# Performance work log

Measured on AMD Instinct MI355X. Metric: run time of the kernel, lower is better.

## Reference

```python
import jax, jax.numpy as jnp
import numpy as np

B, L, D_MODEL = 2, 2048, 1024
EXPAND, D_STATE, D_CONV = 2, 16, 4
D_INNER = EXPAND * D_MODEL
DT_RANK = D_MODEL // 16  # mamba default: ceil(d_model/16)


def setup_inputs() -> dict:
    key = jax.random.key(0)
    ks = jax.random.split(key, 8)
    s = 0.02
    return {
        "x": jax.random.normal(ks[0], (B, L, D_MODEL), jnp.float32),
        "in_proj_w": jax.random.normal(ks[1], (2 * D_INNER, D_MODEL), jnp.float32) * s,
        "conv_w": jax.random.normal(ks[2], (D_INNER, D_CONV), jnp.float32) * s,
        "conv_b": jnp.zeros((D_INNER,), jnp.float32),
        "x_proj_w": jax.random.normal(ks[3], (DT_RANK + 2 * D_STATE, D_INNER), jnp.float32) * s,
        "dt_proj_w": jax.random.normal(ks[4], (D_INNER, DT_RANK), jnp.float32) * s,
        "dt_proj_b": jnp.full((D_INNER,), -4.6, jnp.float32),  # softplus(-4.6) ~ 0.01 dt init
        "A_log": jnp.log(jnp.broadcast_to(jnp.arange(1, D_STATE + 1, dtype=jnp.float32), (D_INNER, D_STATE))),
        "D": jnp.ones((D_INNER,), jnp.float32),
        "ssm_out_w": jax.random.normal(ks[5], (D_MODEL, D_INNER), jnp.float32) * s,
        "final_w": jax.random.normal(ks[6], (D_MODEL, D_MODEL), jnp.float32) * s,
        "final_b": jnp.zeros((D_MODEL,), jnp.float32),
    }


def _forward(x, in_proj_w, conv_w, conv_b, x_proj_w, dt_proj_w, dt_proj_b,
             A_log, D, ssm_out_w, final_w, final_b):
    d_inner, d_state = A_log.shape
    dt_rank = dt_proj_w.shape[1]
    d_conv = conv_w.shape[1]

    # in_proj -> split into x-branch and gate z  (B, L, 2*d_inner)
    xz = jnp.einsum('bld,ed->ble', x, in_proj_w)
    xin, z = jnp.split(xz, 2, axis=-1)

    # causal depthwise conv1d over time, then SiLU
    xc = jax.lax.conv_general_dilated(
        xin.swapaxes(1, 2),               # (B, d_inner, L)
        conv_w[:, None, :],               # (O=d_inner, I/g=1, W=d_conv)
        window_strides=(1,),
        padding=[(d_conv - 1, 0)],
        dimension_numbers=('NCH', 'OIH', 'NCH'),
        feature_group_count=d_inner,
    )
    xc = jax.nn.silu(xc + conv_b[None, :, None]).swapaxes(1, 2)  # (B, L, d_inner)

    # input-dependent SSM parameters
    x_dbl = jnp.einsum('bld,ed->ble', xc, x_proj_w)              # (B, L, dt_rank+2*d_state)
    dt, Bm, Cm = jnp.split(x_dbl, [dt_rank, dt_rank + d_state], axis=-1)
    delta = jax.nn.softplus(jnp.einsum('blr,dr->bld', dt, dt_proj_w) + dt_proj_b)  # (B,L,d_inner)
    A = -jnp.exp(A_log)                                          # (d_inner, d_state)

    # selective scan: h_t = exp(dt*A) h_{t-1} + dt*B_t*u_t ; y_t = <h_t, C_t>
    def step(h, t):
        delta_t, B_t, C_t, u_t = t                               # (B,Di), (B,N), (B,N), (B,Di)
        h = jnp.exp(delta_t[..., None] * A) * h + (delta_t * u_t)[..., None] * B_t[:, None, :]
        return h, jnp.einsum('bdn,bn->bd', h, C_t)

    h0 = jnp.zeros((x.shape[0], d_inner, d_state), x.dtype)
    xs = (delta.swapaxes(0, 1), Bm.swapaxes(0, 1), Cm.swapaxes(0, 1), xc.swapaxes(0, 1))
    _, ys = jax.lax.scan(step, h0, xs)                           # (L, B, d_inner)

    y = ys.swapaxes(0, 1) + xc * D                               # skip term D*u
    y = y * jax.nn.silu(z)                                       # gating
    out = jnp.einsum('bld,md->blm', y, ssm_out_w)                # Mamba out_proj -> d_model
    # wrapper: Linear(d_model, d_model) then SiLU
    return jax.nn.silu(jnp.einsum('blm,nm->bln', out, final_w) + final_b)


def reference(x, in_proj_w, conv_w, conv_b, x_proj_w, dt_proj_w, dt_proj_b,
              A_log, D, ssm_out_w, final_w, final_b):
    return _forward(x, in_proj_w, conv_w, conv_b, x_proj_w, dt_proj_w, dt_proj_b,
                    A_log, D, ssm_out_w, final_w, final_b)
```

## Files before the change

kernel.cpp:

```cpp
#include <hip/hip_runtime.h>
#include <hip/hip_bf16.h>
#include <math.h>

#define BB 2
#define LL 2048
#define DMODEL 1024
#define DINNER 2048
#define DSTATE 16
#define DCONV 4
#define DTRANK 64
#define MROWS (BB * LL)
#define XPROJ_N (DTRANK + 2 * DSTATE)

#define SEG 64
#define LS (LL / SEG)
#define DPB 64

#define XKSPLIT 8
#define XKC (DINNER / XKSPLIT)

typedef unsigned short ushort_t;
typedef short s8v __attribute__((ext_vector_type(8)));
typedef float f4v __attribute__((ext_vector_type(4)));

__device__ __forceinline__ float siluf(float x) {
    return x / (1.f + expf(-x));
}
__device__ __forceinline__ float softplusf(float x) {
    return fmaxf(x, 0.f) + log1pf(expf(-fabsf(x)));
}
__device__ __forceinline__ ushort_t f32_to_bf16(float f) {
    unsigned u = __builtin_bit_cast(unsigned, f);
    unsigned r = (u + 0x7FFFu + ((u >> 16) & 1u)) >> 16;
    return (ushort_t)r;
}
__device__ __forceinline__ float bf16_to_f32(ushort_t u) {
    return __builtin_bit_cast(float, ((unsigned)u) << 16);
}

__global__ __launch_bounds__(256) void prep_kernel(
    const float* __restrict__ x, const float* __restrict__ ipw,
    const float* __restrict__ sow, const float* __restrict__ fw,
    const float* __restrict__ xpw, const float* __restrict__ dtw,
    ushort_t* __restrict__ x_bf, ushort_t* __restrict__ ipw_bf,
    ushort_t* __restrict__ sow_bf, ushort_t* __restrict__ fw_bf,
    ushort_t* __restrict__ xpw_bf, ushort_t* __restrict__ dtw_bf,
    float4* __restrict__ xdbl_zero)
{
    const long i = ((long)blockIdx.x * 256 + threadIdx.x) * 4;
    const float* src; ushort_t* dst; long off;
    if      (i < 4194304L)  { src = x;   dst = x_bf;   off = i; }
    else if (i < 8388608L)  { src = ipw; dst = ipw_bf; off = i - 4194304L; }
    else if (i < 10485760L) { src = sow; dst = sow_bf; off = i - 8388608L; }
    else if (i < 11534336L) { src = fw;  dst = fw_bf;  off = i - 10485760L; }
    else if (i < 11730944L) { src = xpw; dst = xpw_bf; off = i - 11534336L; }
    else if (i < 11862016L) { src = dtw; dst = dtw_bf; off = i - 11730944L; }
    else { xdbl_zero[(i - 11862016L) >> 2] = make_float4(0.f, 0.f, 0.f, 0.f); return; }
    const float4 v = *reinterpret_cast<const float4*>(src + off);
    ushort_t o[4] = {f32_to_bf16(v.x), f32_to_bf16(v.y),
                     f32_to_bf16(v.z), f32_to_bf16(v.w)};
    *reinterpret_cast<uint2*>(dst + off) = *reinterpret_cast<uint2*>(o);
}

__global__ __launch_bounds__(256) void cast_dt_kernel(
    const float* __restrict__ xdbl, ushort_t* __restrict__ dtbf)
{
    const int i4 = (blockIdx.x * 256 + threadIdx.x) * 4;
    const int row = i4 >> 6;
    const int col = i4 & 63;
    const float4 v = *reinterpret_cast<const float4*>(&xdbl[(size_t)row * XPROJ_N + col]);
    ushort_t o[4] = {f32_to_bf16(v.x), f32_to_bf16(v.y),
                     f32_to_bf16(v.z), f32_to_bf16(v.w)};
    *reinterpret_cast<uint2*>(dtbf + i4) = *reinterpret_cast<uint2*>(o);
}

#define TM 128
#define TN 128
#define TBK 32

__global__ __launch_bounds__(512) void gemm_bf16_mfma(
    const ushort_t* __restrict__ A, int lda,
    const ushort_t* __restrict__ B, int ldb,
    int K,
    void* __restrict__ C0v, void* __restrict__ C1v, int splitN, int ldc,
    const float* __restrict__ bias, int act, int store_bf16)
{
    __shared__ __align__(16) ushort_t As[TM * TBK];
    __shared__ __align__(16) ushort_t Bs[TN * TBK];

    const int tid  = threadIdx.x;
    const int lane = tid & 63;
    const int w    = tid >> 6;
    const int wm   = w & 1;
    const int wn   = w >> 1;
    const int m0   = blockIdx.y * TM;
    const int n0   = blockIdx.x * TN;

    const int srow = lane >> 2;
    const int scol = (lane & 3) * 8;

    f4v acc[4][2] = {};

    for (int k0 = 0; k0 < K; k0 += TBK) {
        {
            const ushort_t* ga = A + (size_t)(m0 + w * 16 + srow) * lda + k0 + scol;
            __builtin_amdgcn_global_load_lds(
                (const __attribute__((address_space(1))) unsigned int*)ga,
                (__attribute__((address_space(3))) unsigned int*)(As + w * 512),
                16, 0, 0);
        }
        {
            const ushort_t* gb = B + (size_t)(n0 + w * 16 + srow) * ldb + k0 + scol;
            __builtin_amdgcn_global_load_lds(
                (const __attribute__((address_space(1))) unsigned int*)gb,
                (__attribute__((address_space(3))) unsigned int*)(Bs + w * 512),
                16, 0, 0);
        }
        __syncthreads();

        const int fr = lane & 15;
        const int kg = lane >> 4;
        s8v a[4], b[2];
        #pragma unroll
        for (int t = 0; t < 4; ++t)
            a[t] = *reinterpret_cast<const s8v*>(As + (wm * 64 + t * 16 + fr) * TBK + kg * 8);
        #pragma unroll
        for (int t = 0; t < 2; ++t)
            b[t] = *reinterpret_cast<const s8v*>(Bs + (wn * 32 + t * 16 + fr) * TBK + kg * 8);
        #pragma unroll
        for (int i = 0; i < 4; ++i)
            #pragma unroll
            for (int j = 0; j < 2; ++j)
                acc[i][j] = __builtin_amdgcn_mfma_f32_16x16x32_bf16(
                    a[i], b[j], acc[i][j], 0, 0, 0);
        __syncthreads();
    }

    const int rbase = (lane >> 4) * 4;
    const int cbase = lane & 15;
    #pragma unroll
    for (int i = 0; i < 4; ++i) {
        #pragma unroll
        for (int j = 0; j < 2; ++j) {
            const int row = m0 + wm * 64 + i * 16 + rbase;
            const int col = n0 + wn * 32 + j * 16 + cbase;
            void* Cp = C0v;
            int c2 = col;
            if (C1v && col >= splitN) { Cp = C1v; c2 = col - splitN; }
            const float bv = bias ? bias[col] : 0.f;
            #pragma unroll
            for (int r = 0; r < 4; ++r) {
                float v = acc[i][j][r] + bv;
                if (act == 1) v = siluf(v);
                else if (act == 2) v = softplusf(v);
                if (store_bf16)
                    ((ushort_t*)Cp)[(size_t)(row + r) * ldc + c2] = f32_to_bf16(v);
                else
                    ((float*)Cp)[(size_t)(row + r) * ldc + c2] = v;
            }
        }
    }
}

#define UM 64
#define UN 128

__global__ __launch_bounds__(512) void gemm64_bf16_mfma(
    const ushort_t* __restrict__ A, int lda,
    const ushort_t* __restrict__ B, int ldb,
    int K,
    void* __restrict__ C0v, int ldc,
    const float* __restrict__ bias, int act, int store_bf16)
{
    __shared__ __align__(16) ushort_t As[UM * TBK];
    __shared__ __align__(16) ushort_t Bs[UN * TBK];

    const int tid  = threadIdx.x;
    const int lane = tid & 63;
    const int w    = tid >> 6;
    const int wm   = w & 1;
    const int wn   = w >> 1;
    const int m0   = blockIdx.y * UM;
    const int n0   = blockIdx.x * UN;

    const int srow = lane >> 2;
    const int scol = (lane & 3) * 8;

    f4v acc[2][2] = {};

    for (int k0 = 0; k0 < K; k0 += TBK) {
        if (w < 4) {
            const ushort_t* ga = A + (size_t)(m0 + w * 16 + srow) * lda + k0 + scol;
            __builtin_amdgcn_global_load_lds(
                (const __attribute__((address_space(1))) unsigned int*)ga,
                (__attribute__((address_space(3))) unsigned int*)(As + w * 512),
                16, 0, 0);
        }
        {
            const ushort_t* gb = B + (size_t)(n0 + w * 16 + srow) * ldb + k0 + scol;
            __builtin_amdgcn_global_load_lds(
                (const __attribute__((address_space(1))) unsigned int*)gb,
                (__attribute__((address_space(3))) unsigned int*)(Bs + w * 512),
                16, 0, 0);
        }
        __syncthreads();

        const int fr = lane & 15;
        const int kg = lane >> 4;
        s8v a[2], b[2];
        #pragma unroll
        for (int t = 0; t < 2; ++t)
            a[t] = *reinterpret_cast<const s8v*>(As + (wm * 32 + t * 16 + fr) * TBK + kg * 8);
        #pragma unroll
        for (int t = 0; t < 2; ++t)
            b[t] = *reinterpret_cast<const s8v*>(Bs + (wn * 32 + t * 16 + fr) * TBK + kg * 8);
        #pragma unroll
        for (int i = 0; i < 2; ++i)
            #pragma unroll
            for (int j = 0; j < 2; ++j)
                acc[i][j] = __builtin_amdgcn_mfma_f32_16x16x32_bf16(
                    a[i], b[j], acc[i][j], 0, 0, 0);
        __syncthreads();
    }

    const int rbase = (lane >> 4) * 4;
    const int cbase = lane & 15;
    #pragma unroll
    for (int i = 0; i < 2; ++i) {
        #pragma unroll
        for (int j = 0; j < 2; ++j) {
            const int row = m0 + wm * 32 + i * 16 + rbase;
            const int col = n0 + wn * 32 + j * 16 + cbase;
            const float bv = bias ? bias[col] : 0.f;
            #pragma unroll
            for (int r = 0; r < 4; ++r) {
                float v = acc[i][j][r] + bv;
                if (act == 1) v = siluf(v);
                else if (act == 2) v = softplusf(v);
                if (store_bf16)
                    ((ushort_t*)C0v)[(size_t)(row + r) * ldc + col] = f32_to_bf16(v);
                else
                    ((float*)C0v)[(size_t)(row + r) * ldc + col] = v;
            }
        }
    }
}

__global__ __launch_bounds__(256) void xproj_mfma(
    const ushort_t* __restrict__ A, const ushort_t* __restrict__ Bw,
    float* __restrict__ Cout)
{
    __shared__ __align__(16) ushort_t As[64 * 32];
    __shared__ __align__(16) ushort_t Bs[96 * 32];

    const int tid = threadIdx.x;
    const int lane = tid & 63;
    const int w = tid >> 6;
    const int kbase = blockIdx.x * XKC;
    const int m0 = blockIdx.y * 64;

    const int srow = lane >> 2;
    const int scol = (lane & 3) * 8;

    f4v acc[6] = {};

    for (int k0 = kbase; k0 < kbase + XKC; k0 += 32) {
        {
            const ushort_t* ga = A + (size_t)(m0 + w * 16 + srow) * DINNER + k0 + scol;
            __builtin_amdgcn_global_load_lds(
                (const __attribute__((address_space(1))) unsigned int*)ga,
                (__attribute__((address_space(3))) unsigned int*)(As + (w * 16) * 32),
                16, 0, 0);
        }
        {
            const ushort_t* gb = Bw + (size_t)(w * 16 + srow) * DINNER + k0 + scol;
            __builtin_amdgcn_global_load_lds(
                (const __attribute__((address_space(1))) unsigned int*)gb,
                (__attribute__((address_space(3))) unsigned int*)(Bs + (w * 16) * 32),
                16, 0, 0);
        }
        if (w < 2) {
            const ushort_t* gb = Bw + (size_t)((4 + w) * 16 + srow) * DINNER + k0 + scol;
            __builtin_amdgcn_global_load_lds(
                (const __attribute__((address_space(1))) unsigned int*)gb,
                (__attribute__((address_space(3))) unsigned int*)(Bs + ((4 + w) * 16) * 32),
                16, 0, 0);
        }
        __syncthreads();

        const int fr = lane & 15;
        const int kg = lane >> 4;
        const s8v a = *reinterpret_cast<const s8v*>(As + (w * 16 + fr) * 32 + kg * 8);
        #pragma unroll
        for (int j = 0; j < 6; ++j) {
            const s8v b = *reinterpret_cast<const s8v*>(Bs + (j * 16 + fr) * 32 + kg * 8);
            acc[j] = __builtin_amdgcn_mfma_f32_16x16x32_bf16(a, b, acc[j], 0, 0, 0);
        }
        __syncthreads();
    }

    const int rbase = (lane >> 4) * 4;
    const int cb = lane & 15;
    #pragma unroll
    for (int j = 0; j < 6; ++j)
        #pragma unroll
        for (int r = 0; r < 4; ++r)
            atomicAdd(&Cout[(size_t)(m0 + w * 16 + rbase + r) * XPROJ_N + j * 16 + cb],
                      acc[j][r]);
}

__global__ __launch_bounds__(256) void conv_silu_kernel(
    const ushort_t* __restrict__ xin, const float* __restrict__ w,
    const float* __restrict__ b, ushort_t* __restrict__ xcbf)
{
    const int idx = blockIdx.x * blockDim.x + threadIdx.x;
    const int c = idx % DINNER;
    const int bl = idx / DINNER;
    const int l = bl % LL;
    const int bb = bl / LL;
    if (bb >= BB) return;

    const ushort_t* xp = xin + (size_t)bb * LL * DINNER + c;
    float acc = b[c];
    #pragma unroll
    for (int k = 0; k < DCONV; ++k) {
        const int ll = l - (DCONV - 1) + k;
        if (ll >= 0)
            acc = fmaf(bf16_to_f32(xp[(size_t)ll * DINNER]), w[c * DCONV + k], acc);
    }
    xcbf[idx] = f32_to_bf16(siluf(acc));
}

__global__ __launch_bounds__(256) void scan_part1(
    const ushort_t* __restrict__ delta, const float* __restrict__ xdbl,
    const ushort_t* __restrict__ xc, const float* __restrict__ A_log,
    float* __restrict__ hloc, float* __restrict__ decay)
{
    const int tid = threadIdx.x;
    const int nsub = tid & 3;
    const int d = blockIdx.x * DPB + (tid >> 2);
    const int seg = blockIdx.y;
    const int b = blockIdx.z;
    const int t0 = seg * LS;

    float Ad[4];
    #pragma unroll
    for (int i = 0; i < 4; ++i)
        Ad[i] = -expf(A_log[d * DSTATE + nsub * 4 + i]);

    float h[4] = {};

    const ushort_t* dp = delta + ((size_t)b * LL) * DINNER + d;
    const ushort_t* up = xc    + ((size_t)b * LL) * DINNER + d;
    const float*    xb = xdbl  + ((size_t)b * LL) * XPROJ_N;

    float sum_dl = 0.f;
    for (int t = t0; t < t0 + LS; ++t) {
        const float dl = bf16_to_f32(dp[(size_t)t * DINNER]);
        const float u  = bf16_to_f32(up[(size_t)t * DINNER]);
        const float4 Bv = *reinterpret_cast<const float4*>(
            &xb[t * XPROJ_N + DTRANK + nsub * 4]);
        const float bv[4] = {Bv.x, Bv.y, Bv.z, Bv.w};
        const float dlu = dl * u;
        sum_dl += dl;
        #pragma unroll
        for (int i = 0; i < 4; ++i)
            h[i] = __expf(dl * Ad[i]) * h[i] + dlu * bv[i];
    }

    const size_t base = (((size_t)b * SEG + seg) * DSTATE + nsub * 4) * DINNER + d;
    #pragma unroll
    for (int i = 0; i < 4; ++i) {
        hloc[base + (size_t)i * DINNER]  = h[i];
        decay[base + (size_t)i * DINNER] = __expf(Ad[i] * sum_dl);
    }
}

__global__ __launch_bounds__(256) void scan_combine(
    float* __restrict__ hloc, const float* __restrict__ decay)
{
    const int idx = blockIdx.x * 256 + threadIdx.x;
    const int d = idx % DINNER;
    const int n = (idx / DINNER) % DSTATE;
    const int b = idx / (DINNER * DSTATE);
    if (b >= BB) return;

    float carry = 0.f;
    for (int s = 0; s < SEG; ++s) {
        const size_t off = (((size_t)b * SEG + s) * DSTATE + n) * DINNER + d;
        const float hl = hloc[off];
        hloc[off] = carry;
        carry = decay[off] * carry + hl;
    }
}

__global__ __launch_bounds__(256) void scan_part2(
    const ushort_t* __restrict__ delta, const float* __restrict__ xdbl,
    const ushort_t* __restrict__ xc, const ushort_t* __restrict__ z,
    const float* __restrict__ A_log, const float* __restrict__ Dvec,
    const float* __restrict__ hstart, ushort_t* __restrict__ ybf)
{
    const int tid = threadIdx.x;
    const int nsub = tid & 3;
    const int d = blockIdx.x * DPB + (tid >> 2);
    const int seg = blockIdx.y;
    const int b = blockIdx.z;
    const int t0 = seg * LS;

    float Ad[4];
    #pragma unroll
    for (int i = 0; i < 4; ++i)
        Ad[i] = -expf(A_log[d * DSTATE + nsub * 4 + i]);

    float h[4];
    const size_t hbase = (((size_t)b * SEG + seg) * DSTATE + nsub * 4) * DINNER + d;
    #pragma unroll
    for (int i = 0; i < 4; ++i)
        h[i] = hstart[hbase + (size_t)i * DINNER];

    const float Dd = Dvec[d];
    const ushort_t* dp = delta + ((size_t)b * LL) * DINNER + d;
    const ushort_t* up = xc    + ((size_t)b * LL) * DINNER + d;
    const float*    xb = xdbl  + ((size_t)b * LL) * XPROJ_N;
    const ushort_t* zp = z     + ((size_t)b * LL) * DINNER + d;
    ushort_t*       yp = ybf   + ((size_t)b * LL) * DINNER + d;

    for (int t = t0; t < t0 + LS; ++t) {
        const float dl = bf16_to_f32(dp[(size_t)t * DINNER]);
        const float u  = bf16_to_f32(up[(size_t)t * DINNER]);
        const float zv = bf16_to_f32(zp[(size_t)t * DINNER]);
        const float4 Bv = *reinterpret_cast<const float4*>(
            &xb[t * XPROJ_N + DTRANK + nsub * 4]);
        const float4 Cv = *reinterpret_cast<const float4*>(
            &xb[t * XPROJ_N + DTRANK + DSTATE + nsub * 4]);
        const float bv[4] = {Bv.x, Bv.y, Bv.z, Bv.w};
        const float cv[4] = {Cv.x, Cv.y, Cv.z, Cv.w};
        const float dlu = dl * u;
        float y = 0.f;
        #pragma unroll
        for (int i = 0; i < 4; ++i) {
            h[i] = __expf(dl * Ad[i]) * h[i] + dlu * bv[i];
            y = fmaf(h[i], cv[i], y);
        }
        y += __shfl_xor(y, 1);
        y += __shfl_xor(y, 2);
        if (nsub == 0)
            yp[(size_t)t * DINNER] = f32_to_bf16((y + u * Dd) * siluf(zv));
    }
}

extern "C" void kernel_launch(void* const* d_in, const int* in_sizes, int n_in,
                              void* d_out, int out_size, void* d_ws, size_t ws_size,
                              hipStream_t stream) {
    const float* x         = (const float*)d_in[0];
    const float* in_proj_w = (const float*)d_in[1];
    const float* conv_w    = (const float*)d_in[2];
    const float* conv_b    = (const float*)d_in[3];
    const float* x_proj_w  = (const float*)d_in[4];
    const float* dt_proj_w = (const float*)d_in[5];
    const float* dt_proj_b = (const float*)d_in[6];
    const float* A_log     = (const float*)d_in[7];
    const float* Dvec      = (const float*)d_in[8];
    const float* ssm_out_w = (const float*)d_in[9];
    const float* final_w   = (const float*)d_in[10];
    const float* final_b   = (const float*)d_in[11];
    float* out = (float*)d_out;

    const size_t MB = 1024 * 1024;
    char* base = (char*)d_ws;
    ushort_t* xin_bf   = (ushort_t*)(base);
    ushort_t* z_bf     = (ushort_t*)(base + 16 * MB);
    ushort_t* xc_bf    = (ushort_t*)(base + 32 * MB);
    ushort_t* delta_bf = (ushort_t*)(base + 48 * MB);
    float*    xdbl     = (float*)(base + 64 * MB);
    ushort_t* x_bf     = (ushort_t*)(base + 78 * MB);
    ushort_t* ipw_bf   = (ushort_t*)(base + 86 * MB);
    ushort_t* sow_bf   = (ushort_t*)(base + 94 * MB);
    ushort_t* fw_bf    = (ushort_t*)(base + 98 * MB);
    ushort_t* xpw_bf   = (ushort_t*)(base + 100 * MB);
    ushort_t* dtw_bf   = (ushort_t*)(base + 100 * MB + 512 * 1024);
    ushort_t* dt_bf    = (ushort_t*)(base + 101 * MB);
    ushort_t* y_bf     = (ushort_t*)(base + 102 * MB);
    ushort_t* outb_bf  = (ushort_t*)(base + 118 * MB);
    float* hloc  = (float*)(base);
    float* decay = (float*)(base + 78 * MB);

    prep_kernel<<<11968, 256, 0, stream>>>(
        x, in_proj_w, ssm_out_w, final_w, x_proj_w, dt_proj_w,
        x_bf, ipw_bf, sow_bf, fw_bf, xpw_bf, dtw_bf, (float4*)xdbl);

    gemm_bf16_mfma<<<dim3(2 * DINNER / TN, MROWS / TM), 512, 0, stream>>>(
        x_bf, DMODEL, ipw_bf, DMODEL, DMODEL,
        xin_bf, z_bf, DINNER, DINNER, nullptr, 0, 1);

    conv_silu_kernel<<<(MROWS * DINNER) / 256, 256, 0, stream>>>(
        xin_bf, conv_w, conv_b, xc_bf);

    xproj_mfma<<<dim3(XKSPLIT, MROWS / 64), 256, 0, stream>>>(xc_bf, xpw_bf, xdbl);

    cast_dt_kernel<<<(MROWS * DTRANK / 4) / 256, 256, 0, stream>>>(xdbl, dt_bf);
    gemm64_bf16_mfma<<<dim3(DINNER / UN, MROWS / UM), 512, 0, stream>>>(
        dt_bf, DTRANK, dtw_bf, DTRANK, DTRANK,
        delta_bf, DINNER, dt_proj_b, 2, 1);

    scan_part1<<<dim3(DINNER / DPB, SEG, BB), 256, 0, stream>>>(
        delta_bf, xdbl, xc_bf, A_log, hloc, decay);
    scan_combine<<<(BB * DSTATE * DINNER) / 256, 256, 0, stream>>>(hloc, decay);
    scan_part2<<<dim3(DINNER / DPB, SEG, BB), 256, 0, stream>>>(
        delta_bf, xdbl, xc_bf, z_bf, A_log, Dvec, hloc, y_bf);

    gemm64_bf16_mfma<<<dim3(DMODEL / UN, MROWS / UM), 512, 0, stream>>>(
        y_bf, DINNER, sow_bf, DINNER, DINNER,
        outb_bf, DMODEL, nullptr, 0, 1);

    gemm64_bf16_mfma<<<dim3(DMODEL / UN, MROWS / UM), 512, 0, stream>>>(
        outb_bf, DMODEL, fw_bf, DMODEL, DMODEL,
        out, DMODEL, final_b, 1, 0);
}
```

Before: 417.7 us.

## Assign one thread per channel holding all 16 SSM states in registers

The chunked scan kernels change from four threads per inner channel (each owning 4 states, combined with cross-lane shuffles) to one thread per channel owning all 16 states. This removes the shuffle reduction and the redundant delta/u/z loads across the four sub-lanes, and each thread's memory accesses are coalesced per channel. In exchange the grid shrinks fourfold (8x64x2 blocks of 256 threads) and register pressure per thread rises, which lowers parallelism and occupancy.

```diff
diff --git a/kernel.cpp b/kernel.cpp
--- a/kernel.cpp
+++ b/kernel.cpp
@@ -14,7 +14,6 @@
 
 #define SEG 64
 #define LS (LL / SEG)
-#define DPB 64
 
 #define XKSPLIT 8
 #define XKC (DINNER / XKSPLIT)
@@ -336,19 +335,19 @@
     const ushort_t* __restrict__ xc, const float* __restrict__ A_log,
     float* __restrict__ hloc, float* __restrict__ decay)
 {
-    const int tid = threadIdx.x;
-    const int nsub = tid & 3;
-    const int d = blockIdx.x * DPB + (tid >> 2);
+    const int d = blockIdx.x * 256 + threadIdx.x;
     const int seg = blockIdx.y;
     const int b = blockIdx.z;
     const int t0 = seg * LS;
 
-    float Ad[4];
-    #pragma unroll
-    for (int i = 0; i < 4; ++i)
-        Ad[i] = -expf(A_log[d * DSTATE + nsub * 4 + i]);
-
-    float h[4] = {};
+    float Ad[DSTATE];
+    #pragma unroll
+    for (int n = 0; n < DSTATE; ++n)
+        Ad[n] = -expf(A_log[d * DSTATE + n]);
+
+    float h[DSTATE];
+    #pragma unroll
+    for (int n = 0; n < DSTATE; ++n) h[n] = 0.f;
 
     const ushort_t* dp = delta + ((size_t)b * LL) * DINNER + d;
     const ushort_t* up = xc    + ((size_t)b * LL) * DINNER + d;
@@ -358,21 +357,24 @@
     for (int t = t0; t < t0 + LS; ++t) {
         const float dl = bf16_to_f32(dp[(size_t)t * DINNER]);
         const float u  = bf16_to_f32(up[(size_t)t * DINNER]);
-        const float4 Bv = *reinterpret_cast<const float4*>(
-            &xb[t * XPROJ_N + DTRANK + nsub * 4]);
-        const float bv[4] = {Bv.x, Bv.y, Bv.z, Bv.w};
+        const float4 b0 = *reinterpret_cast<const float4*>(&xb[t * XPROJ_N + DTRANK + 0]);
+        const float4 b1 = *reinterpret_cast<const float4*>(&xb[t * XPROJ_N + DTRANK + 4]);
+        const float4 b2 = *reinterpret_cast<const float4*>(&xb[t * XPROJ_N + DTRANK + 8]);
+        const float4 b3 = *reinterpret_cast<const float4*>(&xb[t * XPROJ_N + DTRANK + 12]);
+        const float Bv[DSTATE] = {b0.x, b0.y, b0.z, b0.w, b1.x, b1.y, b1.z, b1.w,
+                                  b2.x, b2.y, b2.z, b2.w, b3.x, b3.y, b3.z, b3.w};
         const float dlu = dl * u;
         sum_dl += dl;
         #pragma unroll
-        for (int i = 0; i < 4; ++i)
-            h[i] = __expf(dl * Ad[i]) * h[i] + dlu * bv[i];
-    }
-
-    const size_t base = (((size_t)b * SEG + seg) * DSTATE + nsub * 4) * DINNER + d;
-    #pragma unroll
-    for (int i = 0; i < 4; ++i) {
-        hloc[base + (size_t)i * DINNER]  = h[i];
-        decay[base + (size_t)i * DINNER] = __expf(Ad[i] * sum_dl);
+        for (int n = 0; n < DSTATE; ++n)
+            h[n] = __expf(dl * Ad[n]) * h[n] + dlu * Bv[n];
+    }
+
+    const size_t base = (((size_t)b * SEG + seg) * DSTATE) * DINNER + d;
+    #pragma unroll
+    for (int n = 0; n < DSTATE; ++n) {
+        hloc[base + (size_t)n * DINNER]  = h[n];
+        decay[base + (size_t)n * DINNER] = __expf(Ad[n] * sum_dl);
     }
 }
 
@@ -400,23 +402,21 @@
     const float* __restrict__ A_log, const float* __restrict__ Dvec,
     const float* __restrict__ hstart, ushort_t* __restrict__ ybf)
 {
-    const int tid = threadIdx.x;
-    const int nsub = tid & 3;
-    const int d = blockIdx.x * DPB + (tid >> 2);
+    const int d = blockIdx.x * 256 + threadIdx.x;
     const int seg = blockIdx.y;
     const int b = blockIdx.z;
     const int t0 = seg * LS;
 
-    float Ad[4];
-    #pragma unroll
-    for (int i = 0; i < 4; ++i)
-        Ad[i] = -expf(A_log[d * DSTATE + nsub * 4 + i]);
-
-    float h[4];
-    const size_t hbase = (((size_t)b * SEG + seg) * DSTATE + nsub * 4) * DINNER + d;
-    #pragma unroll
-    for (int i = 0; i < 4; ++i)
-        h[i] = hstart[hbase + (size_t)i * DINNER];
+    float Ad[DSTATE];
+    #pragma unroll
+    for (int n = 0; n < DSTATE; ++n)
+        Ad[n] = -expf(A_log[d * DSTATE + n]);
+
+    float h[DSTATE];
+    const size_t hbase = (((size_t)b * SEG + seg) * DSTATE) * DINNER + d;
+    #pragma unroll
+    for (int n = 0; n < DSTATE; ++n)
+        h[n] = hstart[hbase + (size_t)n * DINNER];
 
     const float Dd = Dvec[d];
     const ushort_t* dp = delta + ((size_t)b * LL) * DINNER + d;
@@ -429,23 +429,26 @@
         const float dl = bf16_to_f32(dp[(size_t)t * DINNER]);
         const float u  = bf16_to_f32(up[(size_t)t * DINNER]);
         const float zv = bf16_to_f32(zp[(size_t)t * DINNER]);
-        const float4 Bv = *reinterpret_cast<const float4*>(
-            &xb[t * XPROJ_N + DTRANK + nsub * 4]);
-        const float4 Cv = *reinterpret_cast<const float4*>(
-            &xb[t * XPROJ_N + DTRANK + DSTATE + nsub * 4]);
-        const float bv[4] = {Bv.x, Bv.y, Bv.z, Bv.w};
-        const float cv[4] = {Cv.x, Cv.y, Cv.z, Cv.w};
+        const float4 b0 = *reinterpret_cast<const float4*>(&xb[t * XPROJ_N + DTRANK + 0]);
+        const float4 b1 = *reinterpret_cast<const float4*>(&xb[t * XPROJ_N + DTRANK + 4]);
+        const float4 b2 = *reinterpret_cast<const float4*>(&xb[t * XPROJ_N + DTRANK + 8]);
+        const float4 b3 = *reinterpret_cast<const float4*>(&xb[t * XPROJ_N + DTRANK + 12]);
+        const float4 c0 = *reinterpret_cast<const float4*>(&xb[t * XPROJ_N + DTRANK + DSTATE + 0]);
+        const float4 c1 = *reinterpret_cast<const float4*>(&xb[t * XPROJ_N + DTRANK + DSTATE + 4]);
+        const float4 c2 = *reinterpret_cast<const float4*>(&xb[t * XPROJ_N + DTRANK + DSTATE + 8]);
+        const float4 c3 = *reinterpret_cast<const float4*>(&xb[t * XPROJ_N + DTRANK + DSTATE + 12]);
+        const float Bv[DSTATE] = {b0.x, b0.y, b0.z, b0.w, b1.x, b1.y, b1.z, b1.w,
+                                  b2.x, b2.y, b2.z, b2.w, b3.x, b3.y, b3.z, b3.w};
+        const float Cv[DSTATE] = {c0.x, c0.y, c0.z, c0.w, c1.x, c1.y, c1.z, c1.w,
+                                  c2.x, c2.y, c2.z, c2.w, c3.x, c3.y, c3.z, c3.w};
         const float dlu = dl * u;
         float y = 0.f;
         #pragma unroll
-        for (int i = 0; i < 4; ++i) {
-            h[i] = __expf(dl * Ad[i]) * h[i] + dlu * bv[i];
-            y = fmaf(h[i], cv[i], y);
-        }
-        y += __shfl_xor(y, 1);
-        y += __shfl_xor(y, 2);
-        if (nsub == 0)
-            yp[(size_t)t * DINNER] = f32_to_bf16((y + u * Dd) * siluf(zv));
+        for (int n = 0; n < DSTATE; ++n) {
+            h[n] = __expf(dl * Ad[n]) * h[n] + dlu * Bv[n];
+            y = fmaf(h[n], Cv[n], y);
+        }
+        yp[(size_t)t * DINNER] = f32_to_bf16((y + u * Dd) * siluf(zv));
     }
 }
 
@@ -503,10 +506,10 @@
         dt_bf, DTRANK, dtw_bf, DTRANK, DTRANK,
         delta_bf, DINNER, dt_proj_b, 2, 1);
 
-    scan_part1<<<dim3(DINNER / DPB, SEG, BB), 256, 0, stream>>>(
+    scan_part1<<<dim3(DINNER / 256, SEG, BB), 256, 0, stream>>>(
         delta_bf, xdbl, xc_bf, A_log, hloc, decay);
     scan_combine<<<(BB * DSTATE * DINNER) / 256, 256, 0, stream>>>(hloc, decay);
-    scan_part2<<<dim3(DINNER / DPB, SEG, BB), 256, 0, stream>>>(
+    scan_part2<<<dim3(DINNER / 256, SEG, BB), 256, 0, stream>>>(
         delta_bf, xdbl, xc_bf, z_bf, A_log, Dvec, hloc, y_bf);
 
     gemm64_bf16_mfma<<<dim3(DMODEL / UN, MROWS / UM), 512, 0, stream>>>(
```

New measurement: 378.9 us. -9.3%, faster.
